# Kernel tuning notes

Hardware: AMD Instinct MI355X
Metric: run time of the kernel (lower is better)

Reference implementation:

```python
import jax, jax.numpy as jnp
import numpy as np

N = 30000      # points
E = 400000     # edges
CIN = 16       # input point features
B = 4          # graphs in batch
H, W = 60, 80  # BEV grid


def _mlp_params(key, cin, cout):
    k1, k2 = jax.random.split(key)
    wa = jax.random.normal(k1, (cin, cout), jnp.float32) * np.float32(np.sqrt(2.0 / cin))
    wb = jax.random.normal(k2, (cout, cout), jnp.float32) * np.float32(np.sqrt(2.0 / cout))
    return wa, jnp.zeros((cout,), jnp.float32), wb, jnp.zeros((cout,), jnp.float32)


def setup_inputs() -> dict:
    key = jax.random.key(0)
    ks = jax.random.split(key, 8)
    x = jax.random.normal(ks[0], (N, CIN), jnp.float32)
    r = jax.random.uniform(ks[1], (N, 3), jnp.float32)
    Z = 1.0 + 9.0 * r[:, 2]
    X = (r[:, 0] - 0.5) * 1.2 * Z   # |X/Z| < 0.6 -> mostly inside image
    Y = (r[:, 1] - 0.5) * 0.9 * Z
    pos = jnp.stack([X, Y, Z], axis=1)
    edge_index = jax.random.randint(ks[2], (2, E), 0, N, jnp.int32)
    batch = jnp.sort(jax.random.randint(ks[3], (N,), 0, B, jnp.int32))
    K = jnp.array([[500.0, 0.0, 320.0], [0.0, 500.0, 240.0], [0.0, 0.0, 1.0]], jnp.float32)
    w11, b11, w12, b12 = _mlp_params(ks[4], CIN + 3, 64)
    w21, b21, w22, b22 = _mlp_params(ks[5], 64 + 3, 128)
    w31, b31, w32, b32 = _mlp_params(ks[6], 128 + 3, 256)
    return dict(x=x, pos=pos, K=K,
                w11=w11, b11=b11, w12=w12, b12=b12,
                w21=w21, b21=b21, w22=w22, b22=b22,
                w31=w31, b31=b31, w32=w32, b32=b32,
                edge_index=edge_index, batch=batch)


def _mlp(h, wa, ba, wb, bb):
    return jax.nn.relu(h @ wa + ba) @ wb + bb


def _pointnet_conv(feat, rel, src, dst, wa, ba, wb, bb):
    # PyG PointNetConv: msg = local_nn([x_j, pos_j - pos_i]); max-aggregate at target i
    msg = _mlp(jnp.concatenate([feat[src], rel], axis=1), wa, ba, wb, bb)
    agg = jax.ops.segment_max(msg, dst, num_segments=N)
    return jnp.where(jnp.isfinite(agg), agg, 0.0)  # empty segments -> 0 (PyG fill)


def _points_to_image(feat, pos, batch, K):
    X, Y, Z = pos[:, 0], pos[:, 1], pos[:, 2]
    u = ((K[0, 0] * X / Z + K[0, 2]) / 640.0 * W).astype(jnp.int32)  # trunc like .long()
    v = ((K[1, 1] * Y / Z + K[1, 2]) / 480.0 * H).astype(jnp.int32)
    mask = (u >= 0) & (u < W) & (v >= 0) & (v < H)
    idx = jnp.where(mask, batch * (H * W) + v * W + u, 0)
    contrib = feat * mask[:, None].astype(feat.dtype)
    flat = jnp.zeros((B * H * W, feat.shape[1]), feat.dtype).at[idx].add(contrib)
    return flat.reshape(B, H, W, feat.shape[1]).transpose(0, 3, 1, 2)


def reference(x, pos, K, w11, b11, w12, b12, w21, b21, w22, b22, w31, b31, w32, b32,
              edge_index, batch):
    src, dst = edge_index[0], edge_index[1]
    rel = pos[src] - pos[dst]
    h = _pointnet_conv(x, rel, src, dst, w11, b11, w12, b12)
    h = _pointnet_conv(h, rel, src, dst, w21, b21, w22, b22)
    h = _pointnet_conv(h, rel, src, dst, w31, b31, w32, b32)
    return _points_to_image(h, pos, batch, K)  # [B, 256, H, W]
```

## Files before the change

kernel.cpp:

```cpp
#include <hip/hip_runtime.h>
#include <math.h>

#define NN 30000
#define NE 400000

typedef _Float16 f16;
typedef _Float16 f16x8 __attribute__((ext_vector_type(8)));
typedef _Float16 f16x4 __attribute__((ext_vector_type(4)));
typedef float f32x4 __attribute__((ext_vector_type(4)));

__device__ __forceinline__ void atomic_max_f(float* addr, float v) {
    if (v >= 0.0f) {
        atomicMax((int*)addr, __float_as_int(v));
    } else {
        atomicMin((unsigned int*)addr, __float_as_uint(v));
    }
}

__global__ __launch_bounds__(256) void fill_neg_inf4(float4* p, int n4) {
    int i = blockIdx.x * blockDim.x + threadIdx.x;
    int stride = gridDim.x * blockDim.x;
    const float4 v = {-INFINITY, -INFINITY, -INFINITY, -INFINITY};
    for (; i < n4; i += stride) p[i] = v;
}

__global__ __launch_bounds__(256) void hist_dst(const int* __restrict__ dst,
                                                int* __restrict__ counts) {
    int e = blockIdx.x * 256 + threadIdx.x;
    if (e < NE) atomicAdd(&counts[dst[e]], 1);
}

__global__ __launch_bounds__(1024) void scan_counts(const int* __restrict__ counts,
                                                    int* __restrict__ cursor) {
    __shared__ int lsum[1024];
    const int t = threadIdx.x;
    const int base = t * 30;
    int s = 0;
    for (int i = 0; i < 30; ++i) {
        int idx = base + i;
        if (idx < NN) s += counts[idx];
    }
    lsum[t] = s;
    __syncthreads();
    int acc = s;
    for (int off = 1; off < 1024; off <<= 1) {
        int v = (t >= off) ? lsum[t - off] : 0;
        __syncthreads();
        acc += v;
        lsum[t] = acc;
        __syncthreads();
    }
    int run = acc - s;
    for (int i = 0; i < 30; ++i) {
        int idx = base + i;
        if (idx < NN) { cursor[idx] = run; run += counts[idx]; }
    }
}

__global__ __launch_bounds__(256) void scatter_edges(const int* __restrict__ src,
                                                     const int* __restrict__ dst,
                                                     int* __restrict__ cursor,
                                                     int* __restrict__ srcS,
                                                     int* __restrict__ dstS) {
    int e = blockIdx.x * 256 + threadIdx.x;
    if (e >= NE) return;
    int d = dst[e];
    int p = atomicAdd(&cursor[d], 1);
    srcS[p] = src[e];
    dstS[p] = d;
}

template<int K, int N>
__global__ __launch_bounds__(256) void pack_w(const float* __restrict__ wsrc,
                                              f16* __restrict__ pB) {
    int f = blockIdx.x * 256 + threadIdx.x;
    if (f >= K * N) return;
    int j = f & 7;
    int l = (f >> 3) & 63;
    int rest = f >> 9;
    constexpr int KS = K / 32;
    int ks = rest % KS;
    int nt = rest / KS;
    int k = ks * 32 + ((l >> 4) << 3) + j;
    int n = nt * 16 + (l & 15);
    pB[f] = (f16)wsrc[k * N + n];
}

__global__ __launch_bounds__(256) void cast_f16(const float* __restrict__ w,
                                                f16* __restrict__ o, int n) {
    int i = blockIdx.x * 256 + threadIdx.x;
    if (i < n) o[i] = (f16)w[i];
}

template<int K, int COUT>
__global__ __launch_bounds__(256) void node_linear(const float* __restrict__ feat,
                                                   const float* __restrict__ wa,
                                                   const float* __restrict__ b,
                                                   f16* __restrict__ A) {
    constexpr int NPB = 8;
    constexpr int G   = 256 / COUT;
    constexpr int NPT = NPB / G;
    __shared__ float sf[NPB * K];
    const int node0 = blockIdx.x * NPB;
    for (int idx = threadIdx.x; idx < NPB * K; idx += 256) {
        float v = feat[node0 * K + idx];
        if (!isfinite(v)) v = 0.0f;
        sf[idx] = v;
    }
    __syncthreads();
    const int j  = threadIdx.x % COUT;
    const int g  = threadIdx.x / COUT;
    const int n0 = g * NPT;
    float acc[NPT];
#pragma unroll
    for (int i = 0; i < NPT; i++) acc[i] = 0.0f;
    for (int k = 0; k < K; k++) {
        float w = wa[k * COUT + j];
#pragma unroll
        for (int nn = 0; nn < NPT; nn++)
            acc[nn] = fmaf(sf[(n0 + nn) * K + k], w, acc[nn]);
    }
    const float bj = b[j];
#pragma unroll
    for (int nn = 0; nn < NPT; nn++)
        A[(size_t)(node0 + n0 + nn) * COUT + j] = (f16)(acc[nn] + bj);
}

template<int K, int C>
__global__ __launch_bounds__(256) void node_gemm(const float* __restrict__ feat,
                                                 const f16* __restrict__ pW,
                                                 const float* __restrict__ bias,
                                                 f16* __restrict__ A) {
    constexpr int NTW = C / 64;
    constexpr int KS  = K / 32;
    __shared__ __align__(16) unsigned char smem[64 * K * 2];
    const int tid = threadIdx.x;
    const int node0 = blockIdx.x * 64;

    {
        const int e = tid >> 2, p = tid & 3;
        const bool valid = (node0 + e) < NN;
        const float* frow = feat + (size_t)(node0 + e) * K;
#pragma unroll
        for (int ch = 0; ch < K / 32; ++ch) {
            const int j0 = (ch * 4 + p) * 8;
            f16x8 hv;
#pragma unroll
            for (int jj = 0; jj < 8; ++jj) {
                float v = valid ? frow[j0 + jj] : 0.0f;
                if (!isfinite(v)) v = 0.0f;
                hv[jj] = (f16)v;
            }
            *(f16x8*)(smem + e * (K * 2) + ((j0 * 2) ^ ((e & 7) << 4))) = hv;
        }
    }
    __syncthreads();

    const int w = tid >> 6, l = tid & 63, lr = l & 15, lg = l >> 4;
    f32x4 acc[4][NTW] = {};
#pragma unroll
    for (int ks = 0; ks < KS; ++ks) {
        f16x8 af[4];
#pragma unroll
        for (int m = 0; m < 4; ++m) {
            const int row = m * 16 + lr;
            af[m] = *(const f16x8*)(smem + row * (K * 2)
                     + (((ks * 32 + lg * 8) * 2) ^ ((row & 7) << 4)));
        }
#pragma unroll
        for (int nt = 0; nt < NTW; ++nt) {
            const int ntg = w * NTW + nt;
            f16x8 bf = *(const f16x8*)(pW + ((size_t)(ntg * KS + ks) * 64 + l) * 8);
#pragma unroll
            for (int m = 0; m < 4; ++m)
                acc[m][nt] = __builtin_amdgcn_mfma_f32_16x16x32_f16(af[m], bf, acc[m][nt], 0, 0, 0);
        }
    }
#pragma unroll
    for (int m = 0; m < 4; ++m)
#pragma unroll
        for (int nt = 0; nt < NTW; ++nt) {
            const int col = w * (C / 4) + nt * 16 + lr;
            const float bv = bias[col];
#pragma unroll
            for (int rr = 0; rr < 4; ++rr) {
                const int row = m * 16 + lg * 4 + rr;
                if (node0 + row < NN)
                    A[(size_t)(node0 + row) * C + col] = (f16)(acc[m][nt][rr] + bv);
            }
        }
}

template<int C, int NW>
__global__ __launch_bounds__(NW * 64, 4) void edge_mfma(const f16* __restrict__ Ah,
                                                        const f16* __restrict__ warelh,
                                                        const f16* __restrict__ pB,
                                                        const float* __restrict__ bb,
                                                        const float* __restrict__ pos,
                                                        const int* __restrict__ srcS,
                                                        const int* __restrict__ dstS,
                                                        float* __restrict__ agg) {
    constexpr int TE   = 64;
    constexpr int BLK  = NW * 64;
    constexpr int CW   = C / NW;
    constexpr int NTW  = CW / 16;
    constexpr int KS   = C / 32;
    constexpr int CPR  = C / 8;
    constexpr int LOGCPR = (C == 256) ? 5 : (C == 128 ? 4 : 3);
    constexpr int CH   = (TE * CPR) / BLK;
    static_assert(NTW >= 1 && CH >= 2, "geometry");

    __shared__ __align__(16) unsigned char h1[TE * C * 2];
    __shared__ __align__(16) f16 s_warel[3 * C];
    __shared__ __align__(8)  f16 s_rel[TE][4];
    __shared__ int s_dst[TE];

    const int tid = threadIdx.x;
    const int nwg = gridDim.x;
    const int q8 = nwg >> 3, r8 = nwg & 7;
    const int xcd = blockIdx.x & 7, o = blockIdx.x >> 3;
    const int bid = (xcd < r8 ? xcd * (q8 + 1) : r8 * (q8 + 1) + (xcd - r8) * q8) + o;
    const int e0 = bid * TE;

    const int slot = tid & (CPR - 1);
    int sv[CH];
    f16x8 av[CH];
#pragma unroll
    for (int i = 0; i < CH; ++i)
        sv[i] = srcS[e0 + ((i * BLK + tid) >> LOGCPR)];
    av[0] = *(const f16x8*)(Ah + (size_t)sv[0] * C + slot * 8);
    av[1] = *(const f16x8*)(Ah + (size_t)sv[1] * C + slot * 8);

    if (tid < TE) {
        int s = srcS[e0 + tid], d = dstS[e0 + tid];
        s_dst[tid] = d;
        s_rel[tid][0] = (f16)(pos[3 * s + 0] - pos[3 * d + 0]);
        s_rel[tid][1] = (f16)(pos[3 * s + 1] - pos[3 * d + 1]);
        s_rel[tid][2] = (f16)(pos[3 * s + 2] - pos[3 * d + 2]);
        s_rel[tid][3] = (f16)0.f;
    }
    for (int i = tid; i < 3 * C / 8; i += BLK)
        ((f16x8*)s_warel)[i] = ((const f16x8*)warelh)[i];
    __syncthreads();

    {
        const f16* wp = s_warel + slot * 8;
        const f16x8 w0 = *(const f16x8*)(wp);
        const f16x8 w1 = *(const f16x8*)(wp + C);
        const f16x8 w2 = *(const f16x8*)(wp + 2 * C);
#pragma unroll
        for (int i = 0; i < CH; ++i) {
            if (i + 2 < CH)
                av[i + 2] = *(const f16x8*)(Ah + (size_t)sv[i + 2] * C + slot * 8);
            const int row = (i * BLK + tid) >> LOGCPR;
            const f16x4 rl = *(const f16x4*)&s_rel[row][0];
            const f16 rx = rl[0], ry = rl[1], rz = rl[2];
            const f16x8 rxv = {rx, rx, rx, rx, rx, rx, rx, rx};
            const f16x8 ryv = {ry, ry, ry, ry, ry, ry, ry, ry};
            const f16x8 rzv = {rz, rz, rz, rz, rz, rz, rz, rz};
            f16x8 hv = av[i] + rxv * w0 + ryv * w1 + rzv * w2;
#pragma unroll
            for (int jj = 0; jj < 8; ++jj)
                hv[jj] = hv[jj] > (f16)0.f ? hv[jj] : (f16)0.f;
            *(f16x8*)(h1 + row * (2 * C) + ((slot * 16) ^ ((row & 7) << 4))) = hv;
        }
    }
    __syncthreads();

    const int w = tid >> 6, l = tid & 63, lr = l & 15, lg = l >> 4;
    f32x4 acc[4][NTW] = {};
    __builtin_amdgcn_s_setprio(1);
#pragma unroll
    for (int ks = 0; ks < KS; ++ks) {
        f16x8 af[4];
#pragma unroll
        for (int m = 0; m < 4; ++m) {
            const int row = m * 16 + lr;
            af[m] = *(const f16x8*)(h1 + row * (2 * C)
                     + (((ks * 32 + lg * 8) * 2) ^ ((row & 7) << 4)));
        }
#pragma unroll
        for (int nt = 0; nt < NTW; ++nt) {
            f16x8 bf = *(const f16x8*)(pB + ((size_t)((w * NTW + nt) * KS + ks) * 64 + l) * 8);
#pragma unroll
            for (int m = 0; m < 4; ++m)
                acc[m][nt] = __builtin_amdgcn_mfma_f32_16x16x32_f16(af[m], bf, acc[m][nt], 0, 0, 0);
        }
    }
    __builtin_amdgcn_s_setprio(0);

    float bbv[NTW];
#pragma unroll
    for (int nt = 0; nt < NTW; ++nt) bbv[nt] = bb[w * CW + nt * 16 + lr];

    const int myd = s_dst[l];
    const int pd  = s_dst[l == 0 ? 0 : l - 1];
    unsigned long long m = __ballot((l == 0) || (myd != pd));

    while (m) {
        const int a = __builtin_ctzll(m);
        const unsigned long long m2 = m & (m - 1);
        const int b = m2 ? __builtin_ctzll(m2) : 64;
        m = m2;
        const int d = s_dst[a];
        const bool interior = (a > 0) && (b < 64);
#pragma unroll
        for (int nt = 0; nt < NTW; ++nt) {
            float v = -INFINITY;
#pragma unroll
            for (int mm = 0; mm < 4; ++mm) {
                if (b <= mm * 16 || a >= mm * 16 + 16) continue;
#pragma unroll
                for (int rr = 0; rr < 4; ++rr) {
                    const int row = mm * 16 + lg * 4 + rr;
                    const bool in = (row >= a) && (row < b);
                    v = fmaxf(v, in ? acc[mm][nt][rr] : -INFINITY);
                }
            }
            v = fmaxf(v, __shfl_xor(v, 16, 64));
            v = fmaxf(v, __shfl_xor(v, 32, 64));
            if (lg == 0) {
                float* addr = &agg[(size_t)d * C + w * CW + nt * 16 + lr];
                if (interior) *addr = v + bbv[nt];
                else          atomic_max_f(addr, v + bbv[nt]);
            }
        }
    }
}

__global__ __launch_bounds__(256) void scatter_img(const float* __restrict__ feat,
                                                   const float* __restrict__ pos,
                                                   const float* __restrict__ Km,
                                                   const int* __restrict__ batch,
                                                   float* __restrict__ img) {
    const int n0 = blockIdx.x * 8;
    const int c = threadIdx.x;
    const float k00 = Km[0], k02 = Km[2], k11 = Km[4], k12 = Km[5];
#pragma unroll
    for (int k = 0; k < 8; ++k) {
        const int n = n0 + k;
        const float X = pos[3 * n + 0], Y = pos[3 * n + 1], Z = pos[3 * n + 2];
        const int u = (int)((k00 * X / Z + k02) / 640.0f * 80.0f);
        const int v = (int)((k11 * Y / Z + k12) / 480.0f * 60.0f);
        if (u < 0 || u >= 80 || v < 0 || v >= 60) continue;
        const int p = (batch[n] * 60 + v) * 80 + u;
        float val = feat[(size_t)n * 256 + c];
        if (!isfinite(val)) val = 0.0f;
        atomicAdd(img + (size_t)p * 256 + c, val);
    }
}

__global__ __launch_bounds__(256) void transpose_img(const float* __restrict__ img,
                                                     float* __restrict__ out) {
    __shared__ float tile[32][33];
    const int b = blockIdx.z;
    const int p0 = blockIdx.x * 32, c0 = blockIdx.y * 32;
    const float* src = img + (size_t)b * 4800 * 256;
    float* dst = out + (size_t)b * 256 * 4800;
    const int tx = threadIdx.x & 31, ty = threadIdx.x >> 5;
#pragma unroll
    for (int i = 0; i < 32; i += 8)
        tile[ty + i][tx] = src[(size_t)(p0 + ty + i) * 256 + c0 + tx];
    __syncthreads();
#pragma unroll
    for (int i = 0; i < 32; i += 8)
        dst[(size_t)(c0 + ty + i) * 4800 + p0 + tx] = tile[tx][ty + i];
}

extern "C" void kernel_launch(void* const* d_in, const int* in_sizes, int n_in,
                              void* d_out, int out_size, void* d_ws, size_t ws_size,
                              hipStream_t stream) {
    const float* x   = (const float*)d_in[0];
    const float* pos = (const float*)d_in[1];
    const float* Km  = (const float*)d_in[2];
    const float* w11 = (const float*)d_in[3];
    const float* b11 = (const float*)d_in[4];
    const float* w12 = (const float*)d_in[5];
    const float* b12 = (const float*)d_in[6];
    const float* w21 = (const float*)d_in[7];
    const float* b21 = (const float*)d_in[8];
    const float* w22 = (const float*)d_in[9];
    const float* b22 = (const float*)d_in[10];
    const float* w31 = (const float*)d_in[11];
    const float* b31 = (const float*)d_in[12];
    const float* w32 = (const float*)d_in[13];
    const float* b32 = (const float*)d_in[14];
    const int* edge  = (const int*)d_in[15];
    const int* batch = (const int*)d_in[16];
    const int* srcp = edge;
    const int* dstp = edge + NE;
    float* out = (float*)d_out;

    float* aggA  = (float*)d_ws;
    float* aggB  = aggA + (size_t)NN * 256;
    f16*   Ah    = (f16*)(aggB + (size_t)NN * 256);
    int*   srcS  = (int*)(Ah + (size_t)NN * 256);
    int*   dstS  = srcS + NE;
    int*   counts = dstS + NE;
    int*   cursor = counts + NN;
    f16*   pW1   = (f16*)(cursor + NN);
    f16*   pW2   = pW1 + 64 * 64;
    f16*   pW3   = pW2 + 128 * 128;
    f16*   pW2n  = pW3 + 256 * 256;
    f16*   pW3n  = pW2n + 64 * 128;
    f16*   wr1   = pW3n + 128 * 256;
    f16*   wr2   = wr1 + 3 * 64;
    f16*   wr3   = wr2 + 3 * 128;

    hipMemsetAsync(counts, 0, NN * sizeof(int), stream);
    hist_dst<<<(NE + 255) / 256, 256, 0, stream>>>(dstp, counts);
    scan_counts<<<1, 1024, 0, stream>>>(counts, cursor);
    scatter_edges<<<(NE + 255) / 256, 256, 0, stream>>>(srcp, dstp, cursor, srcS, dstS);

    pack_w<64, 64><<<(64 * 64 + 255) / 256, 256, 0, stream>>>(w12, pW1);
    pack_w<128, 128><<<(128 * 128 + 255) / 256, 256, 0, stream>>>(w22, pW2);
    pack_w<256, 256><<<(256 * 256 + 255) / 256, 256, 0, stream>>>(w32, pW3);
    pack_w<64, 128><<<(64 * 128 + 255) / 256, 256, 0, stream>>>(w21, pW2n);
    pack_w<128, 256><<<(128 * 256 + 255) / 256, 256, 0, stream>>>(w31, pW3n);
    cast_f16<<<1, 256, 0, stream>>>(w11 + 16 * 64, wr1, 3 * 64);
    cast_f16<<<2, 256, 0, stream>>>(w21 + 64 * 128, wr2, 3 * 128);
    cast_f16<<<3, 256, 0, stream>>>(w31 + 128 * 256, wr3, 3 * 256);

    node_linear<16, 64><<<NN / 8, 256, 0, stream>>>(x, w11, b11, Ah);
    fill_neg_inf4<<<512, 256, 0, stream>>>((float4*)aggB, NN * 64 / 4);
    edge_mfma<64, 4><<<NE / 64, 256, 0, stream>>>(Ah, wr1, pW1, b12,
                                                  pos, srcS, dstS, aggB);
    node_gemm<64, 128><<<(NN + 63) / 64, 256, 0, stream>>>(aggB, pW2n, b21, Ah);
    fill_neg_inf4<<<512, 256, 0, stream>>>((float4*)aggA, NN * 128 / 4);
    edge_mfma<128, 8><<<NE / 64, 512, 0, stream>>>(Ah, wr2, pW2, b22,
                                                   pos, srcS, dstS, aggA);
    node_gemm<128, 256><<<(NN + 63) / 64, 256, 0, stream>>>(aggA, pW3n, b31, Ah);
    fill_neg_inf4<<<512, 256, 0, stream>>>((float4*)aggB, NN * 256 / 4);
    edge_mfma<256, 8><<<NE / 64, 512, 0, stream>>>(Ah, wr3, pW3, b32,
                                                   pos, srcS, dstS, aggB);
    hipMemsetAsync(aggA, 0, (size_t)4 * 4800 * 256 * sizeof(float), stream);
    scatter_img<<<NN / 8, 256, 0, stream>>>(aggB, pos, Km, batch, aggA);
    transpose_img<<<dim3(150, 8, 4), 256, 0, stream>>>(aggA, out);
}
```

Baseline: 381.1 us.

## Process several edge tiles per block with software-pipelined gather and double-buffered LDS

Each edge_mfma block now loops over four 64-edge tiles instead of one. While it works on the current tile, it issues the global gathers (source features, relative positions, destinations) for the next tile. The hidden-activation LDS buffer is doubled and the rel/dst buffers are tripled so the next tile's staging does not race with the current tile's MFMA and segment-max. The weight slice and bias loads are hoisted out of the tile loop. This is meant to hide gather latency behind MFMA work and to amortise per-block setup, at the cost of more LDS per block, fewer resident blocks per CU, and a grid four times smaller.

```diff
diff --git a/kernel.cpp b/kernel.cpp
--- a/kernel.cpp
+++ b/kernel.cpp
@@ -199,7 +199,8 @@
                                                         const float* __restrict__ pos,
                                                         const int* __restrict__ srcS,
                                                         const int* __restrict__ dstS,
-                                                        float* __restrict__ agg) {
+                                                        float* __restrict__ agg,
+                                                        int NT, int TT) {
     constexpr int TE   = 64;
     constexpr int BLK  = NW * 64;
     constexpr int CW   = C / NW;
@@ -210,119 +211,146 @@
     constexpr int CH   = (TE * CPR) / BLK;
     static_assert(NTW >= 1 && CH >= 2, "geometry");
 
-    __shared__ __align__(16) unsigned char h1[TE * C * 2];
+    __shared__ __align__(16) unsigned char h1[2][TE * C * 2];
     __shared__ __align__(16) f16 s_warel[3 * C];
-    __shared__ __align__(8)  f16 s_rel[TE][4];
-    __shared__ int s_dst[TE];
+    __shared__ __align__(8)  f16 s_rel[3][TE][4];
+    __shared__ int s_dst[3][TE];
 
     const int tid = threadIdx.x;
     const int nwg = gridDim.x;
     const int q8 = nwg >> 3, r8 = nwg & 7;
     const int xcd = blockIdx.x & 7, o = blockIdx.x >> 3;
     const int bid = (xcd < r8 ? xcd * (q8 + 1) : r8 * (q8 + 1) + (xcd - r8) * q8) + o;
-    const int e0 = bid * TE;
+
+    const int t0 = bid * NT;
+    int tcount = TT - t0;
+    if (tcount <= 0) return;
+    if (tcount > NT) tcount = NT;
 
     const int slot = tid & (CPR - 1);
+    const int w = tid >> 6, l = tid & 63, lr = l & 15, lg = l >> 4;
+
+    for (int i = tid; i < 3 * C / 8; i += BLK)
+        ((f16x8*)s_warel)[i] = ((const f16x8*)warelh)[i];
+
+    float bbv[NTW];
+#pragma unroll
+    for (int nt = 0; nt < NTW; ++nt) bbv[nt] = bb[w * CW + nt * 16 + lr];
+
     int sv[CH];
     f16x8 av[CH];
-#pragma unroll
-    for (int i = 0; i < CH; ++i)
-        sv[i] = srcS[e0 + ((i * BLK + tid) >> LOGCPR)];
-    av[0] = *(const f16x8*)(Ah + (size_t)sv[0] * C + slot * 8);
-    av[1] = *(const f16x8*)(Ah + (size_t)sv[1] * C + slot * 8);
 
     if (tid < TE) {
-        int s = srcS[e0 + tid], d = dstS[e0 + tid];
-        s_dst[tid] = d;
-        s_rel[tid][0] = (f16)(pos[3 * s + 0] - pos[3 * d + 0]);
-        s_rel[tid][1] = (f16)(pos[3 * s + 1] - pos[3 * d + 1]);
-        s_rel[tid][2] = (f16)(pos[3 * s + 2] - pos[3 * d + 2]);
-        s_rel[tid][3] = (f16)0.f;
-    }
-    for (int i = tid; i < 3 * C / 8; i += BLK)
-        ((f16x8*)s_warel)[i] = ((const f16x8*)warelh)[i];
+        int s = srcS[t0 * TE + tid], d = dstS[t0 * TE + tid];
+        s_dst[0][tid] = d;
+        s_rel[0][tid][0] = (f16)(pos[3 * s + 0] - pos[3 * d + 0]);
+        s_rel[0][tid][1] = (f16)(pos[3 * s + 1] - pos[3 * d + 1]);
+        s_rel[0][tid][2] = (f16)(pos[3 * s + 2] - pos[3 * d + 2]);
+        s_rel[0][tid][3] = (f16)0.f;
+    }
+#pragma unroll
+    for (int i = 0; i < CH; ++i) {
+        sv[i] = srcS[t0 * TE + ((i * BLK + tid) >> LOGCPR)];
+        av[i] = *(const f16x8*)(Ah + (size_t)sv[i] * C + slot * 8);
+    }
     __syncthreads();
 
-    {
-        const f16* wp = s_warel + slot * 8;
-        const f16x8 w0 = *(const f16x8*)(wp);
-        const f16x8 w1 = *(const f16x8*)(wp + C);
-        const f16x8 w2 = *(const f16x8*)(wp + 2 * C);
-#pragma unroll
-        for (int i = 0; i < CH; ++i) {
-            if (i + 2 < CH)
-                av[i + 2] = *(const f16x8*)(Ah + (size_t)sv[i + 2] * C + slot * 8);
-            const int row = (i * BLK + tid) >> LOGCPR;
-            const f16x4 rl = *(const f16x4*)&s_rel[row][0];
-            const f16 rx = rl[0], ry = rl[1], rz = rl[2];
-            const f16x8 rxv = {rx, rx, rx, rx, rx, rx, rx, rx};
-            const f16x8 ryv = {ry, ry, ry, ry, ry, ry, ry, ry};
-            const f16x8 rzv = {rz, rz, rz, rz, rz, rz, rz, rz};
-            f16x8 hv = av[i] + rxv * w0 + ryv * w1 + rzv * w2;
-#pragma unroll
-            for (int jj = 0; jj < 8; ++jj)
-                hv[jj] = hv[jj] > (f16)0.f ? hv[jj] : (f16)0.f;
-            *(f16x8*)(h1 + row * (2 * C) + ((slot * 16) ^ ((row & 7) << 4))) = hv;
-        }
-    }
-    __syncthreads();
-
-    const int w = tid >> 6, l = tid & 63, lr = l & 15, lg = l >> 4;
-    f32x4 acc[4][NTW] = {};
-    __builtin_amdgcn_s_setprio(1);
-#pragma unroll
-    for (int ks = 0; ks < KS; ++ks) {
-        f16x8 af[4];
-#pragma unroll
-        for (int m = 0; m < 4; ++m) {
-            const int row = m * 16 + lr;
-            af[m] = *(const f16x8*)(h1 + row * (2 * C)
-                     + (((ks * 32 + lg * 8) * 2) ^ ((row & 7) << 4)));
-        }
-#pragma unroll
-        for (int nt = 0; nt < NTW; ++nt) {
-            f16x8 bf = *(const f16x8*)(pB + ((size_t)((w * NTW + nt) * KS + ks) * 64 + l) * 8);
-#pragma unroll
-            for (int m = 0; m < 4; ++m)
-                acc[m][nt] = __builtin_amdgcn_mfma_f32_16x16x32_f16(af[m], bf, acc[m][nt], 0, 0, 0);
-        }
-    }
-    __builtin_amdgcn_s_setprio(0);
-
-    float bbv[NTW];
-#pragma unroll
-    for (int nt = 0; nt < NTW; ++nt) bbv[nt] = bb[w * CW + nt * 16 + lr];
-
-    const int myd = s_dst[l];
-    const int pd  = s_dst[l == 0 ? 0 : l - 1];
-    unsigned long long m = __ballot((l == 0) || (myd != pd));
-
-    while (m) {
-        const int a = __builtin_ctzll(m);
-        const unsigned long long m2 = m & (m - 1);
-        const int b = m2 ? __builtin_ctzll(m2) : 64;
-        m = m2;
-        const int d = s_dst[a];
-        const bool interior = (a > 0) && (b < 64);
-#pragma unroll
-        for (int nt = 0; nt < NTW; ++nt) {
-            float v = -INFINITY;
-#pragma unroll
-            for (int mm = 0; mm < 4; ++mm) {
-                if (b <= mm * 16 || a >= mm * 16 + 16) continue;
-#pragma unroll
-                for (int rr = 0; rr < 4; ++rr) {
-                    const int row = mm * 16 + lg * 4 + rr;
-                    const bool in = (row >= a) && (row < b);
-                    v = fmaxf(v, in ? acc[mm][nt][rr] : -INFINITY);
+    for (int tt = 0; tt < tcount; ++tt) {
+        const int mb = tt % 3;
+        const int hb = tt & 1;
+
+        {
+            const f16* wp = s_warel + slot * 8;
+            const f16x8 w0 = *(const f16x8*)(wp);
+            const f16x8 w1 = *(const f16x8*)(wp + C);
+            const f16x8 w2 = *(const f16x8*)(wp + 2 * C);
+#pragma unroll
+            for (int i = 0; i < CH; ++i) {
+                const int row = (i * BLK + tid) >> LOGCPR;
+                const f16x4 rl = *(const f16x4*)&s_rel[mb][row][0];
+                const f16 rx = rl[0], ry = rl[1], rz = rl[2];
+                const f16x8 rxv = {rx, rx, rx, rx, rx, rx, rx, rx};
+                const f16x8 ryv = {ry, ry, ry, ry, ry, ry, ry, ry};
+                const f16x8 rzv = {rz, rz, rz, rz, rz, rz, rz, rz};
+                f16x8 hv = av[i] + rxv * w0 + ryv * w1 + rzv * w2;
+#pragma unroll
+                for (int jj = 0; jj < 8; ++jj)
+                    hv[jj] = hv[jj] > (f16)0.f ? hv[jj] : (f16)0.f;
+                *(f16x8*)(h1[hb] + row * (2 * C) + ((slot * 16) ^ ((row & 7) << 4))) = hv;
+            }
+        }
+
+        if (tt + 1 < tcount) {
+            const int tn = t0 + tt + 1;
+            const int mn = (tt + 1) % 3;
+            if (tid < TE) {
+                int s = srcS[tn * TE + tid], d = dstS[tn * TE + tid];
+                s_dst[mn][tid] = d;
+                s_rel[mn][tid][0] = (f16)(pos[3 * s + 0] - pos[3 * d + 0]);
+                s_rel[mn][tid][1] = (f16)(pos[3 * s + 1] - pos[3 * d + 1]);
+                s_rel[mn][tid][2] = (f16)(pos[3 * s + 2] - pos[3 * d + 2]);
+                s_rel[mn][tid][3] = (f16)0.f;
+            }
+#pragma unroll
+            for (int i = 0; i < CH; ++i) {
+                sv[i] = srcS[tn * TE + ((i * BLK + tid) >> LOGCPR)];
+                av[i] = *(const f16x8*)(Ah + (size_t)sv[i] * C + slot * 8);
+            }
+        }
+        __syncthreads();
+
+        f32x4 acc[4][NTW] = {};
+        __builtin_amdgcn_s_setprio(1);
+#pragma unroll
+        for (int ks = 0; ks < KS; ++ks) {
+            f16x8 af[4];
+#pragma unroll
+            for (int m = 0; m < 4; ++m) {
+                const int row = m * 16 + lr;
+                af[m] = *(const f16x8*)(h1[hb] + row * (2 * C)
+                         + (((ks * 32 + lg * 8) * 2) ^ ((row & 7) << 4)));
+            }
+#pragma unroll
+            for (int nt = 0; nt < NTW; ++nt) {
+                f16x8 bf = *(const f16x8*)(pB + ((size_t)((w * NTW + nt) * KS + ks) * 64 + l) * 8);
+#pragma unroll
+                for (int m = 0; m < 4; ++m)
+                    acc[m][nt] = __builtin_amdgcn_mfma_f32_16x16x32_f16(af[m], bf, acc[m][nt], 0, 0, 0);
+            }
+        }
+        __builtin_amdgcn_s_setprio(0);
+
+        const int myd = s_dst[mb][l];
+        const int pd  = s_dst[mb][l == 0 ? 0 : l - 1];
+        unsigned long long m = __ballot((l == 0) || (myd != pd));
+
+        while (m) {
+            const int a = __builtin_ctzll(m);
+            const unsigned long long m2 = m & (m - 1);
+            const int b = m2 ? __builtin_ctzll(m2) : 64;
+            m = m2;
+            const int d = s_dst[mb][a];
+            const bool interior = (a > 0) && (b < 64);
+#pragma unroll
+            for (int nt = 0; nt < NTW; ++nt) {
+                float v = -INFINITY;
+#pragma unroll
+                for (int mm = 0; mm < 4; ++mm) {
+                    if (b <= mm * 16 || a >= mm * 16 + 16) continue;
+#pragma unroll
+                    for (int rr = 0; rr < 4; ++rr) {
+                        const int row = mm * 16 + lg * 4 + rr;
+                        const bool in = (row >= a) && (row < b);
+                        v = fmaxf(v, in ? acc[mm][nt][rr] : -INFINITY);
+                    }
                 }
-            }
-            v = fmaxf(v, __shfl_xor(v, 16, 64));
-            v = fmaxf(v, __shfl_xor(v, 32, 64));
-            if (lg == 0) {
-                float* addr = &agg[(size_t)d * C + w * CW + nt * 16 + lr];
-                if (interior) *addr = v + bbv[nt];
-                else          atomic_max_f(addr, v + bbv[nt]);
+                v = fmaxf(v, __shfl_xor(v, 16, 64));
+                v = fmaxf(v, __shfl_xor(v, 32, 64));
+                if (lg == 0) {
+                    float* addr = &agg[(size_t)d * C + w * CW + nt * 16 + lr];
+                    if (interior) *addr = v + bbv[nt];
+                    else          atomic_max_f(addr, v + bbv[nt]);
+                }
             }
         }
     }
@@ -421,18 +449,22 @@
     cast_f16<<<2, 256, 0, stream>>>(w21 + 64 * 128, wr2, 3 * 128);
     cast_f16<<<3, 256, 0, stream>>>(w31 + 128 * 256, wr3, 3 * 256);
 
+    const int TT = NE / 64;
+    const int NT = 4;
+    const int EG = (TT + NT - 1) / NT;
+
     node_linear<16, 64><<<NN / 8, 256, 0, stream>>>(x, w11, b11, Ah);
     fill_neg_inf4<<<512, 256, 0, stream>>>((float4*)aggB, NN * 64 / 4);
-    edge_mfma<64, 4><<<NE / 64, 256, 0, stream>>>(Ah, wr1, pW1, b12,
-                                                  pos, srcS, dstS, aggB);
+    edge_mfma<64, 4><<<EG, 256, 0, stream>>>(Ah, wr1, pW1, b12,
+                                             pos, srcS, dstS, aggB, NT, TT);
     node_gemm<64, 128><<<(NN + 63) / 64, 256, 0, stream>>>(aggB, pW2n, b21, Ah);
     fill_neg_inf4<<<512, 256, 0, stream>>>((float4*)aggA, NN * 128 / 4);
-    edge_mfma<128, 8><<<NE / 64, 512, 0, stream>>>(Ah, wr2, pW2, b22,
-                                                   pos, srcS, dstS, aggA);
+    edge_mfma<128, 8><<<EG, 512, 0, stream>>>(Ah, wr2, pW2, b22,
+                                              pos, srcS, dstS, aggA, NT, TT);
     node_gemm<128, 256><<<(NN + 63) / 64, 256, 0, stream>>>(aggA, pW3n, b31, Ah);
     fill_neg_inf4<<<512, 256, 0, stream>>>((float4*)aggB, NN * 256 / 4);
-    edge_mfma<256, 8><<<NE / 64, 512, 0, stream>>>(Ah, wr3, pW3, b32,
-                                                   pos, srcS, dstS, aggB);
+    edge_mfma<256, 8><<<EG, 512, 0, stream>>>(Ah, wr3, pW3, b32,
+                                              pos, srcS, dstS, aggB, NT, TT);
     hipMemsetAsync(aggA, 0, (size_t)4 * 4800 * 256 * sizeof(float), stream);
     scatter_img<<<NN / 8, 256, 0, stream>>>(aggB, pos, Km, batch, aggA);
     transpose_img<<<dim3(150, 8, 4), 256, 0, stream>>>(aggA, out);
```

New measurement: 516.0 us. 35.4% more time.

## Pad per-destination edge lists into 16-row groups aligned to MFMA tiles

Applied to the files above, without the earlier changes.

Edges sorted by destination are now padded so each destination owns whole groups of 16 rows. Each MFMA 16-row block then maps to exactly one node, with per-group node, count and exclusivity metadata. This replaces the ballot-based segment walk in the epilogue with a fixed per-block reduction, and nodes covered by a single group are written with a plain store instead of an atomic max. In exchange, padding inflates the number of rows gathered and multiplied, launches more blocks (extra ones exit early), and adds memsets plus a metadata-building kernel.

```diff
diff --git a/kernel.cpp b/kernel.cpp
--- a/kernel.cpp
+++ b/kernel.cpp
@@ -3,6 +3,8 @@
 
 #define NN 30000
 #define NE 400000
+#define GMAX 55040
+#define TMAX 13760
 
 typedef _Float16 f16;
 typedef _Float16 f16x8 __attribute__((ext_vector_type(8)));
@@ -30,15 +32,17 @@
     if (e < NE) atomicAdd(&counts[dst[e]], 1);
 }
 
-__global__ __launch_bounds__(1024) void scan_counts(const int* __restrict__ counts,
-                                                    int* __restrict__ cursor) {
+__global__ __launch_bounds__(1024) void scan_groups(const int* __restrict__ counts,
+                                                    int* __restrict__ goff,
+                                                    int* __restrict__ cursor,
+                                                    int* __restrict__ gTot) {
     __shared__ int lsum[1024];
     const int t = threadIdx.x;
     const int base = t * 30;
     int s = 0;
     for (int i = 0; i < 30; ++i) {
         int idx = base + i;
-        if (idx < NN) s += counts[idx];
+        if (idx < NN) s += (counts[idx] + 15) >> 4;
     }
     lsum[t] = s;
     __syncthreads();
@@ -53,21 +57,43 @@
     int run = acc - s;
     for (int i = 0; i < 30; ++i) {
         int idx = base + i;
-        if (idx < NN) { cursor[idx] = run; run += counts[idx]; }
-    }
-}
-
-__global__ __launch_bounds__(256) void scatter_edges(const int* __restrict__ src,
-                                                     const int* __restrict__ dst,
-                                                     int* __restrict__ cursor,
-                                                     int* __restrict__ srcS,
-                                                     int* __restrict__ dstS) {
+        if (idx < NN) {
+            goff[idx] = run;
+            cursor[idx] = run * 16;
+            run += (counts[idx] + 15) >> 4;
+        }
+    }
+    if (t == 1023) gTot[0] = acc;
+}
+
+__global__ __launch_bounds__(256) void build_meta(const int* __restrict__ counts,
+                                                  const int* __restrict__ goff,
+                                                  int* __restrict__ gnode,
+                                                  int* __restrict__ gcnt,
+                                                  int* __restrict__ gexcl) {
+    int n = blockIdx.x * 256 + threadIdx.x;
+    if (n >= NN) return;
+    int c = counts[n];
+    if (c == 0) return;
+    int g0 = goff[n];
+    int gpn = (c + 15) >> 4;
+    for (int k = 0; k < gpn; ++k) {
+        int rem = c - 16 * k;
+        gnode[g0 + k] = n;
+        gcnt[g0 + k] = rem > 16 ? 16 : rem;
+        gexcl[g0 + k] = (gpn == 1) ? 1 : 0;
+    }
+}
+
+__global__ __launch_bounds__(256) void scatter_pad(const int* __restrict__ src,
+                                                   const int* __restrict__ dst,
+                                                   int* __restrict__ cursor,
+                                                   int* __restrict__ srcP) {
     int e = blockIdx.x * 256 + threadIdx.x;
     if (e >= NE) return;
     int d = dst[e];
     int p = atomicAdd(&cursor[d], 1);
-    srcS[p] = src[e];
-    dstS[p] = d;
+    srcP[p] = src[e];
 }
 
 template<int K, int N>
@@ -197,8 +223,11 @@
                                                         const f16* __restrict__ pB,
                                                         const float* __restrict__ bb,
                                                         const float* __restrict__ pos,
-                                                        const int* __restrict__ srcS,
-                                                        const int* __restrict__ dstS,
+                                                        const int* __restrict__ srcP,
+                                                        const int* __restrict__ gnode,
+                                                        const int* __restrict__ gcnt,
+                                                        const int* __restrict__ gexcl,
+                                                        const int* __restrict__ gTot,
                                                         float* __restrict__ agg) {
     constexpr int TE   = 64;
     constexpr int BLK  = NW * 64;
@@ -213,27 +242,35 @@
     __shared__ __align__(16) unsigned char h1[TE * C * 2];
     __shared__ __align__(16) f16 s_warel[3 * C];
     __shared__ __align__(8)  f16 s_rel[TE][4];
-    __shared__ int s_dst[TE];
+    __shared__ int s_gn[4], s_gc[4], s_ge[4];
 
     const int tid = threadIdx.x;
     const int nwg = gridDim.x;
     const int q8 = nwg >> 3, r8 = nwg & 7;
     const int xcd = blockIdx.x & 7, o = blockIdx.x >> 3;
     const int bid = (xcd < r8 ? xcd * (q8 + 1) : r8 * (q8 + 1) + (xcd - r8) * q8) + o;
-    const int e0 = bid * TE;
+
+    const int g0 = bid * 4;
+    if (g0 >= gTot[0]) return;
+    const int r0 = bid * TE;
 
     const int slot = tid & (CPR - 1);
     int sv[CH];
     f16x8 av[CH];
 #pragma unroll
     for (int i = 0; i < CH; ++i)
-        sv[i] = srcS[e0 + ((i * BLK + tid) >> LOGCPR)];
+        sv[i] = srcP[r0 + ((i * BLK + tid) >> LOGCPR)];
     av[0] = *(const f16x8*)(Ah + (size_t)sv[0] * C + slot * 8);
     av[1] = *(const f16x8*)(Ah + (size_t)sv[1] * C + slot * 8);
 
+    if (tid < 4) {
+        s_gn[tid] = gnode[g0 + tid];
+        s_gc[tid] = gcnt[g0 + tid];
+        s_ge[tid] = gexcl[g0 + tid];
+    }
     if (tid < TE) {
-        int s = srcS[e0 + tid], d = dstS[e0 + tid];
-        s_dst[tid] = d;
+        int s = srcP[r0 + tid];
+        int d = gnode[g0 + (tid >> 4)];
         s_rel[tid][0] = (f16)(pos[3 * s + 0] - pos[3 * d + 0]);
         s_rel[tid][1] = (f16)(pos[3 * s + 1] - pos[3 * d + 1]);
         s_rel[tid][2] = (f16)(pos[3 * s + 2] - pos[3 * d + 2]);
@@ -293,36 +330,28 @@
 #pragma unroll
     for (int nt = 0; nt < NTW; ++nt) bbv[nt] = bb[w * CW + nt * 16 + lr];
 
-    const int myd = s_dst[l];
-    const int pd  = s_dst[l == 0 ? 0 : l - 1];
-    unsigned long long m = __ballot((l == 0) || (myd != pd));
-
-    while (m) {
-        const int a = __builtin_ctzll(m);
-        const unsigned long long m2 = m & (m - 1);
-        const int b = m2 ? __builtin_ctzll(m2) : 64;
-        m = m2;
-        const int d = s_dst[a];
-        const bool interior = (a > 0) && (b < 64);
+#pragma unroll
+    for (int m = 0; m < 4; ++m) {
+        const int cnt = s_gc[m];
+        if (cnt == 0) continue;
+        const int node = s_gn[m];
+        const bool excl = s_ge[m] != 0;
+        bool ok[4];
+#pragma unroll
+        for (int rr = 0; rr < 4; ++rr) ok[rr] = (lg * 4 + rr) < cnt;
 #pragma unroll
         for (int nt = 0; nt < NTW; ++nt) {
             float v = -INFINITY;
 #pragma unroll
-            for (int mm = 0; mm < 4; ++mm) {
-                if (b <= mm * 16 || a >= mm * 16 + 16) continue;
-#pragma unroll
-                for (int rr = 0; rr < 4; ++rr) {
-                    const int row = mm * 16 + lg * 4 + rr;
-                    const bool in = (row >= a) && (row < b);
-                    v = fmaxf(v, in ? acc[mm][nt][rr] : -INFINITY);
-                }
-            }
+            for (int rr = 0; rr < 4; ++rr)
+                v = fmaxf(v, ok[rr] ? acc[m][nt][rr] : -INFINITY);
             v = fmaxf(v, __shfl_xor(v, 16, 64));
             v = fmaxf(v, __shfl_xor(v, 32, 64));
             if (lg == 0) {
-                float* addr = &agg[(size_t)d * C + w * CW + nt * 16 + lr];
-                if (interior) *addr = v + bbv[nt];
-                else          atomic_max_f(addr, v + bbv[nt]);
+                float* addr = &agg[(size_t)node * C + w * CW + nt * 16 + lr];
+                const float outv = v + bbv[nt];
+                if (excl) *addr = outv;
+                else      atomic_max_f(addr, outv);
             }
         }
     }
@@ -394,11 +423,15 @@
     float* aggA  = (float*)d_ws;
     float* aggB  = aggA + (size_t)NN * 256;
     f16*   Ah    = (f16*)(aggB + (size_t)NN * 256);
-    int*   srcS  = (int*)(Ah + (size_t)NN * 256);
-    int*   dstS  = srcS + NE;
-    int*   counts = dstS + NE;
-    int*   cursor = counts + NN;
-    f16*   pW1   = (f16*)(cursor + NN);
+    int*   srcP  = (int*)(Ah + (size_t)NN * 256);
+    int*   counts = srcP + (size_t)TMAX * 64;
+    int*   goff   = counts + NN;
+    int*   cursor = goff + NN;
+    int*   gTot   = cursor + NN;
+    int*   gnode  = gTot + 16;
+    int*   gcnt   = gnode + GMAX;
+    int*   gexcl  = gcnt + GMAX;
+    f16*   pW1   = (f16*)(gexcl + GMAX);
     f16*   pW2   = pW1 + 64 * 64;
     f16*   pW3   = pW2 + 128 * 128;
     f16*   pW2n  = pW3 + 256 * 256;
@@ -408,9 +441,13 @@
     f16*   wr3   = wr2 + 3 * 128;
 
     hipMemsetAsync(counts, 0, NN * sizeof(int), stream);
+    hipMemsetAsync(srcP, 0, (size_t)TMAX * 64 * sizeof(int), stream);
+    hipMemsetAsync(gnode, 0, GMAX * sizeof(int), stream);
+    hipMemsetAsync(gcnt, 0, GMAX * sizeof(int), stream);
     hist_dst<<<(NE + 255) / 256, 256, 0, stream>>>(dstp, counts);
-    scan_counts<<<1, 1024, 0, stream>>>(counts, cursor);
-    scatter_edges<<<(NE + 255) / 256, 256, 0, stream>>>(srcp, dstp, cursor, srcS, dstS);
+    scan_groups<<<1, 1024, 0, stream>>>(counts, goff, cursor, gTot);
+    build_meta<<<(NN + 255) / 256, 256, 0, stream>>>(counts, goff, gnode, gcnt, gexcl);
+    scatter_pad<<<(NE + 255) / 256, 256, 0, stream>>>(srcp, dstp, cursor, srcP);
 
     pack_w<64, 64><<<(64 * 64 + 255) / 256, 256, 0, stream>>>(w12, pW1);
     pack_w<128, 128><<<(128 * 128 + 255) / 256, 256, 0, stream>>>(w22, pW2);
@@ -423,16 +460,16 @@
 
     node_linear<16, 64><<<NN / 8, 256, 0, stream>>>(x, w11, b11, Ah);
     fill_neg_inf4<<<512, 256, 0, stream>>>((float4*)aggB, NN * 64 / 4);
-    edge_mfma<64, 4><<<NE / 64, 256, 0, stream>>>(Ah, wr1, pW1, b12,
-                                                  pos, srcS, dstS, aggB);
+    edge_mfma<64, 4><<<TMAX, 256, 0, stream>>>(Ah, wr1, pW1, b12, pos,
+                                               srcP, gnode, gcnt, gexcl, gTot, aggB);
     node_gemm<64, 128><<<(NN + 63) / 64, 256, 0, stream>>>(aggB, pW2n, b21, Ah);
     fill_neg_inf4<<<512, 256, 0, stream>>>((float4*)aggA, NN * 128 / 4);
-    edge_mfma<128, 8><<<NE / 64, 512, 0, stream>>>(Ah, wr2, pW2, b22,
-                                                   pos, srcS, dstS, aggA);
+    edge_mfma<128, 8><<<TMAX, 512, 0, stream>>>(Ah, wr2, pW2, b22, pos,
+                                                srcP, gnode, gcnt, gexcl, gTot, aggA);
     node_gemm<128, 256><<<(NN + 63) / 64, 256, 0, stream>>>(aggA, pW3n, b31, Ah);
     fill_neg_inf4<<<512, 256, 0, stream>>>((float4*)aggB, NN * 256 / 4);
-    edge_mfma<256, 8><<<NE / 64, 512, 0, stream>>>(Ah, wr3, pW3, b32,
-                                                   pos, srcS, dstS, aggB);
+    edge_mfma<256, 8><<<TMAX, 512, 0, stream>>>(Ah, wr3, pW3, b32, pos,
+                                                srcP, gnode, gcnt, gexcl, gTot, aggB);
     hipMemsetAsync(aggA, 0, (size_t)4 * 4800 * 256 * sizeof(float), stream);
     scatter_img<<<NN / 8, 256, 0, stream>>>(aggB, pos, Km, batch, aggA);
     transpose_img<<<dim3(150, 8, 4), 256, 0, stream>>>(aggA, out);
```

Measured after the change: 519.0 us. 36.2% more time.
